# Optimization experiments

Measured on AMD Instinct MI355X. Metric: run time of the kernel, lower is better.

Reference implementation:

```python
import jax, jax.numpy as jnp
import numpy as np

SCALE_CLS = 7.0
EPS = 1e-12

def _l2norm(x):
    # torch F.normalize: x / max(||x||_2, eps) along last dim
    n = jnp.sqrt(jnp.sum(x * x, axis=-1, keepdims=True))
    return x / jnp.maximum(n, EPS)

def setup_inputs() -> dict:
    key = jax.random.key(0)
    k1, k2 = jax.random.split(key)
    B, Q, C, D, H, W = 4, 75, 5, 512, 6, 6
    ftrain = jax.random.normal(k1, (B, Q, C, D, H, W), dtype=jnp.float32)
    ftest = jax.random.normal(k2, (B, Q, C, D, H, W), dtype=jnp.float32)
    return {"ftrain": ftrain, "ftest": ftest, "K": 28}

def reference(ftrain, ftest, K):
    B, Q, C, D, H, W = ftrain.shape
    P = H * W  # 36 spatial positions
    # spatial means -> [B,Q,C,1,D]
    ftest_mean = ftest.mean(axis=(4, 5))[:, :, :, None, :]
    ftrain_mean = ftrain.mean(axis=(4, 5))[:, :, :, None, :]
    # flatten spatial, move channel last -> [B,Q,C,P,D]
    ft = jnp.swapaxes(ftest.reshape(B, Q, C, D, P), 3, 4)
    fr = jnp.swapaxes(ftrain.reshape(B, Q, C, D, P), 3, 4)
    ft = _l2norm(ft)
    fr = _l2norm(fr)
    ftest_mean = _l2norm(ftest_mean)
    ftrain_mean = _l2norm(ftrain_mean)
    # global scores [B,Q,C]
    scores = SCALE_CLS * jnp.sum(jnp.squeeze(ftest_mean * ftrain_mean), axis=-1)
    # per-position scores [B,Q,C,P]
    ftrain_scores = SCALE_CLS * jnp.sum(ftest_mean * fr, axis=-1)
    ftest_scores = SCALE_CLS * jnp.sum(ft * ftrain_mean, axis=-1)
    # top-K positions (indices distinct, so one-hot-sum mask == gather)
    _, train_ind = jax.lax.top_k(ftrain_scores, K)  # [B,Q,C,K]
    _, test_ind = jax.lax.top_k(ftest_scores, K)
    # gather top-K spatial features and average -> [B,Q,C,D]
    ftest_fuse = jnp.take_along_axis(ft, test_ind[..., None], axis=3).sum(axis=3) / K
    ftrain_fuse = jnp.take_along_axis(fr, train_ind[..., None], axis=3).sum(axis=3) / K
    ftest_fuse = _l2norm(ftest_fuse)
    ftrain_fuse = _l2norm(ftrain_fuse)
    scores_final = SCALE_CLS * jnp.sum(ftest_fuse * ftrain_fuse, axis=-1)
    return (scores, scores_final)
```

## Files before the change

### kernel.cpp

```cpp
#include <hip/hip_runtime.h>
#include <stdint.h>

#define NGRP 1500
#define DD   512
#define PP   36
#define DP   (DD*PP)
#define SCALE_CLS 7.0f
#define EPS 1e-12f

__device__ __forceinline__ float waveRed(float x){
  #pragma unroll
  for (int off = 32; off; off >>= 1) x += __shfl_xor(x, off, 64);
  return x;
}

__global__ __launch_bounds__(512)
void topk_fuse(const float* __restrict__ gtrain,
               const float* __restrict__ gtest,
               const int* __restrict__ Kp,
               float* __restrict__ out)
{
  __shared__ float sT[DP];
  __shared__ float sR[DP];
  __shared__ float s_tm[DD], s_rm[DD];
  __shared__ __align__(16) float s_q[PP];
  __shared__ __align__(16) float s_e[PP];
  __shared__ __align__(16) float s_a[PP];
  __shared__ __align__(16) float s_b[PP];
  __shared__ __align__(16) float s_wt[PP];
  __shared__ __align__(16) float s_wr[PP];
  __shared__ float s_nt[PP], s_nr[PP];
  __shared__ float s_st[PP], s_sr[PP];
  __shared__ float s_red[24];

  const int t    = threadIdx.x;
  const int lane = t & 63;
  const int wave = t >> 6;
  const int g    = blockIdx.x;
  const int K    = Kp[0];

  const char* gT = (const char*)(gtest  + (size_t)g * DP);
  const char* gR = (const char*)(gtrain + (size_t)g * DP);
  char* sTc = (char*)sT;
  char* sRc = (char*)sR;

  if (t < PP) { s_q[t] = 0.f; s_e[t] = 0.f; s_a[t] = 0.f; s_b[t] = 0.f; }

  {
    const int base = wave * 9216;
    #pragma unroll
    for (int s = 0; s < 9; ++s) {
      const int off = base + s * 1024;
      __builtin_amdgcn_global_load_lds((const uint32_t*)(gT + off + lane*16),
                                       (uint32_t*)(sTc + off), 16, 0, 0);
    }
    #pragma unroll
    for (int s = 0; s < 9; ++s) {
      const int off = base + s * 1024;
      __builtin_amdgcn_global_load_lds((const uint32_t*)(gR + off + lane*16),
                                       (uint32_t*)(sRc + off), 16, 0, 0);
    }
  }

  asm volatile("s_waitcnt vmcnt(9) lgkmcnt(0)" ::: "memory");
  __builtin_amdgcn_s_barrier();
  __builtin_amdgcn_sched_barrier(0);

  float tm;
  {
    const float4* r4 = (const float4*)(sT + t * PP);
    float s = 0.f;
    #pragma unroll
    for (int j = 0; j < 9; ++j) {
      float4 x = r4[j];
      s += (x.x + x.y) + (x.z + x.w);
    }
    tm = s * (1.0f / 36.0f);
    s_tm[t] = tm;
  }
  {
    float pm2 = waveRed(tm * tm);
    if (lane == 0) s_red[wave] = pm2;
  }

  if (t < 504) {
    const int p = t % 36, c = t / 36;
    float q = 0.f;
    for (int d = c; d < DD; d += 14) { float x = sT[d*PP + p]; q += x * x; }
    atomicAdd(&s_q[p], q);
  }

  asm volatile("s_waitcnt vmcnt(0) lgkmcnt(0)" ::: "memory");
  __builtin_amdgcn_s_barrier();
  __builtin_amdgcn_sched_barrier(0);

  float rm;
  {
    const float4* r4 = (const float4*)(sR + t * PP);
    float s = 0.f;
    #pragma unroll
    for (int j = 0; j < 9; ++j) {
      float4 x = r4[j];
      s += (x.x + x.y) + (x.z + x.w);
    }
    rm = s * (1.0f / 36.0f);
    s_rm[t] = rm;
  }
  {
    float pr2 = waveRed(rm * rm);
    float pmr = waveRed(rm * tm);
    if (lane == 0) { s_red[8 + wave] = pr2; s_red[16 + wave] = pmr; }
  }
  __syncthreads();

  if (t == 0) {
    float m2 = 0.f, r2 = 0.f, mr = 0.f;
    #pragma unroll
    for (int w = 0; w < 8; ++w) {
      m2 += s_red[w]; r2 += s_red[8 + w]; mr += s_red[16 + w];
    }
    out[g] = SCALE_CLS * mr / (fmaxf(sqrtf(m2), EPS) * fmaxf(sqrtf(r2), EPS));
  }

  if (t < 504) {
    const int p = t % 36, c = t / 36;
    float a = 0.f, e = 0.f, b = 0.f;
    for (int d = c; d < DD; d += 14) {
      const int i = d * PP + p;
      float x = sT[i], y = sR[i];
      a += x * s_rm[d];
      e += y * y;
      b += y * s_tm[d];
    }
    atomicAdd(&s_a[p], a); atomicAdd(&s_e[p], e); atomicAdd(&s_b[p], b);
  }
  __syncthreads();

  if (wave < 2 && lane < PP) {
    const float* qq = wave ? s_e : s_q;
    const float* dm = wave ? s_b : s_a;
    float n  = fmaxf(sqrtf(qq[lane]), EPS);
    float sc = dm[lane] / n;
    if (wave) { s_nr[lane] = n; s_sr[lane] = sc; }
    else      { s_nt[lane] = n; s_st[lane] = sc; }
  }
  __syncthreads();

  if (wave < 2 && lane < PP) {
    const float* sc = wave ? s_sr : s_st;
    const float* nn = wave ? s_nr : s_nt;
    float*       w  = wave ? s_wr : s_wt;
    float mine = sc[lane];
    int rank = 0;
    #pragma unroll
    for (int p = 0; p < PP; ++p) {
      float o = sc[p];
      rank += ((o > mine) || (o == mine && p < lane)) ? 1 : 0;
    }
    w[lane] = (rank < K) ? (1.0f / nn[lane]) : 0.f;
  }
  __syncthreads();

  {
    const float4* rt = (const float4*)(sT + t * PP);
    const float4* rr = (const float4*)(sR + t * PP);
    const float4* w4t = (const float4*)s_wt;
    const float4* w4r = (const float4*)s_wr;
    float U = 0.f, V = 0.f;
    #pragma unroll
    for (int j = 0; j < 9; ++j) {
      float4 x = rt[j], y = rr[j], a4 = w4t[j], b4 = w4r[j];
      U += x.x*a4.x + x.y*a4.y + x.z*a4.z + x.w*a4.w;
      V += y.x*b4.x + y.y*b4.y + y.z*b4.z + y.w*b4.w;
    }
    float u2 = waveRed(U * U);
    float v2 = waveRed(V * V);
    float uv = waveRed(U * V);
    if (lane == 0) { s_red[wave] = u2; s_red[8 + wave] = v2; s_red[16 + wave] = uv; }
  }
  __syncthreads();
  if (t == 0) {
    float u2 = 0.f, v2 = 0.f, uv = 0.f;
    #pragma unroll
    for (int w = 0; w < 8; ++w) {
      u2 += s_red[w]; v2 += s_red[8 + w]; uv += s_red[16 + w];
    }
    out[NGRP + g] = SCALE_CLS * uv / (fmaxf(sqrtf(u2), EPS) * fmaxf(sqrtf(v2), EPS));
  }
}

extern "C" void kernel_launch(void* const* d_in, const int* in_sizes, int n_in,
                              void* d_out, int out_size, void* d_ws, size_t ws_size,
                              hipStream_t stream)
{
  const float* ftrain = (const float*)d_in[0];
  const float* ftest  = (const float*)d_in[1];
  const int*   Kp     = (const int*)d_in[2];
  float*       out    = (float*)d_out;
  topk_fuse<<<NGRP, 512, 0, stream>>>(ftrain, ftest, Kp, out);
}
```

Measured before the change: 271.3 us.

## Use persistent blocks with register prefetch of next group's features

Replaces one-block-per-group launch with 256 persistent blocks that loop over groups, prefetching the next group's test and train tiles into registers while computing the current one from LDS. It also merges the per-position norm and dot reductions into one pass and computes both means together. The aim is to hide global-memory latency behind compute, since LDS usage allows only one block per CU. In exchange it uses many registers per thread and adds an explicit register-to-LDS copy each iteration.

```diff
diff --git a/kernel.cpp b/kernel.cpp
--- a/kernel.cpp
+++ b/kernel.cpp
@@ -5,6 +5,9 @@
 #define DD   512
 #define PP   36
 #define DP   (DD*PP)
+#define NB   256
+#define NT   512
+#define QPT  9
 #define SCALE_CLS 7.0f
 #define EPS 1e-12f
 
@@ -14,178 +17,149 @@
   return x;
 }
 
-__global__ __launch_bounds__(512)
-void topk_fuse(const float* __restrict__ gtrain,
-               const float* __restrict__ gtest,
-               const int* __restrict__ Kp,
-               float* __restrict__ out)
+__global__ __launch_bounds__(NT, 2)
+void topk_fuse(const float* gtrain, const float* gtest,
+               const int* Kp, float* out)
 {
   __shared__ float sT[DP];
   __shared__ float sR[DP];
   __shared__ float s_tm[DD], s_rm[DD];
-  __shared__ __align__(16) float s_q[PP];
-  __shared__ __align__(16) float s_e[PP];
-  __shared__ __align__(16) float s_a[PP];
-  __shared__ __align__(16) float s_b[PP];
+  __shared__ float s_q[PP], s_e[PP];
+  __shared__ float s_a[PP], s_b[PP];
+  __shared__ float s_nt[PP], s_nr[PP];
+  __shared__ float s_st[PP], s_sr[PP];
   __shared__ __align__(16) float s_wt[PP];
   __shared__ __align__(16) float s_wr[PP];
-  __shared__ float s_nt[PP], s_nr[PP];
-  __shared__ float s_st[PP], s_sr[PP];
   __shared__ float s_red[24];
 
   const int t    = threadIdx.x;
   const int lane = t & 63;
   const int wave = t >> 6;
-  const int g    = blockIdx.x;
+  const int b    = blockIdx.x;
   const int K    = Kp[0];
+  const int nj   = (NGRP - b + NB - 1) / NB;
 
-  const char* gT = (const char*)(gtest  + (size_t)g * DP);
-  const char* gR = (const char*)(gtrain + (size_t)g * DP);
-  char* sTc = (char*)sT;
-  char* sRc = (char*)sR;
-
+  float4 pT[QPT], pR[QPT];
+  {
+    const float4* gT4 = (const float4*)(gtest  + (size_t)b * DP);
+    const float4* gR4 = (const float4*)(gtrain + (size_t)b * DP);
+    #pragma unroll
+    for (int s = 0; s < QPT; ++s) pT[s] = gT4[t + NT*s];
+    #pragma unroll
+    for (int s = 0; s < QPT; ++s) pR[s] = gR4[t + NT*s];
+  }
   if (t < PP) { s_q[t] = 0.f; s_e[t] = 0.f; s_a[t] = 0.f; s_b[t] = 0.f; }
 
-  {
-    const int base = wave * 9216;
+  for (int j = 0; j < nj; ++j) {
+    const int g = b + NB * j;
+
+    float4* sT4 = (float4*)sT;
+    float4* sR4 = (float4*)sR;
     #pragma unroll
-    for (int s = 0; s < 9; ++s) {
-      const int off = base + s * 1024;
-      __builtin_amdgcn_global_load_lds((const uint32_t*)(gT + off + lane*16),
-                                       (uint32_t*)(sTc + off), 16, 0, 0);
+    for (int s = 0; s < QPT; ++s) sT4[t + NT*s] = pT[s];
+    #pragma unroll
+    for (int s = 0; s < QPT; ++s) sR4[t + NT*s] = pR[s];
+
+    if (j + 1 < nj) {
+      const int g2 = g + NB;
+      const float4* gT4 = (const float4*)(gtest  + (size_t)g2 * DP);
+      const float4* gR4 = (const float4*)(gtrain + (size_t)g2 * DP);
+      #pragma unroll
+      for (int s = 0; s < QPT; ++s) pT[s] = gT4[t + NT*s];
+      #pragma unroll
+      for (int s = 0; s < QPT; ++s) pR[s] = gR4[t + NT*s];
     }
+    __builtin_amdgcn_sched_barrier(0);
+    __syncthreads();
+
+    const float4* rt4 = (const float4*)(sT + t * PP);
+    const float4* rr4 = (const float4*)(sR + t * PP);
+    float st = 0.f, sr = 0.f;
     #pragma unroll
-    for (int s = 0; s < 9; ++s) {
-      const int off = base + s * 1024;
-      __builtin_amdgcn_global_load_lds((const uint32_t*)(gR + off + lane*16),
-                                       (uint32_t*)(sRc + off), 16, 0, 0);
+    for (int i = 0; i < 9; ++i) {
+      float4 x = rt4[i], y = rr4[i];
+      st += (x.x + x.y) + (x.z + x.w);
+      sr += (y.x + y.y) + (y.z + y.w);
     }
-  }
+    const float tm = st * (1.0f/36.0f), rm = sr * (1.0f/36.0f);
+    s_tm[t] = tm; s_rm[t] = rm;
+    {
+      float pm2 = waveRed(tm * tm);
+      float pr2 = waveRed(rm * rm);
+      float pmr = waveRed(tm * rm);
+      if (lane == 0) { s_red[wave] = pm2; s_red[8+wave] = pr2; s_red[16+wave] = pmr; }
+    }
+    __syncthreads();
 
-  asm volatile("s_waitcnt vmcnt(9) lgkmcnt(0)" ::: "memory");
-  __builtin_amdgcn_s_barrier();
-  __builtin_amdgcn_sched_barrier(0);
+    if (t == 0) {
+      float m2 = 0.f, r2 = 0.f, mr = 0.f;
+      #pragma unroll
+      for (int w = 0; w < 8; ++w) { m2 += s_red[w]; r2 += s_red[8+w]; mr += s_red[16+w]; }
+      out[g] = SCALE_CLS * mr / (fmaxf(sqrtf(m2), EPS) * fmaxf(sqrtf(r2), EPS));
+    }
 
-  float tm;
-  {
-    const float4* r4 = (const float4*)(sT + t * PP);
-    float s = 0.f;
-    #pragma unroll
-    for (int j = 0; j < 9; ++j) {
-      float4 x = r4[j];
-      s += (x.x + x.y) + (x.z + x.w);
+    if (t < 504) {
+      const int p = t % 36, c = t / 36;
+      float q = 0.f, e = 0.f, a = 0.f, bb = 0.f;
+      for (int d = c; d < DD; d += 14) {
+        const int i = d * PP + p;
+        float x = sT[i], y = sR[i];
+        q += x * x;        e += y * y;
+        a += x * s_rm[d];  bb += y * s_tm[d];
+      }
+      atomicAdd(&s_q[p], q);  atomicAdd(&s_e[p], e);
+      atomicAdd(&s_a[p], a);  atomicAdd(&s_b[p], bb);
     }
-    tm = s * (1.0f / 36.0f);
-    s_tm[t] = tm;
-  }
-  {
-    float pm2 = waveRed(tm * tm);
-    if (lane == 0) s_red[wave] = pm2;
-  }
+    __syncthreads();
 
-  if (t < 504) {
-    const int p = t % 36, c = t / 36;
-    float q = 0.f;
-    for (int d = c; d < DD; d += 14) { float x = sT[d*PP + p]; q += x * x; }
-    atomicAdd(&s_q[p], q);
-  }
+    if (wave < 2 && lane < PP) {
+      const float* qq = wave ? s_e : s_q;
+      const float* dm = wave ? s_b : s_a;
+      float n  = fmaxf(sqrtf(qq[lane]), EPS);
+      float sc = dm[lane] / n;
+      if (wave) { s_nr[lane] = n; s_sr[lane] = sc; }
+      else      { s_nt[lane] = n; s_st[lane] = sc; }
+    }
+    __syncthreads();
 
-  asm volatile("s_waitcnt vmcnt(0) lgkmcnt(0)" ::: "memory");
-  __builtin_amdgcn_s_barrier();
-  __builtin_amdgcn_sched_barrier(0);
+    if (wave < 2 && lane < PP) {
+      const float* sc = wave ? s_sr : s_st;
+      const float* nn = wave ? s_nr : s_nt;
+      float*       w  = wave ? s_wr : s_wt;
+      float mine = sc[lane];
+      int rank = 0;
+      #pragma unroll
+      for (int p = 0; p < PP; ++p) {
+        float o = sc[p];
+        rank += ((o > mine) || (o == mine && p < lane)) ? 1 : 0;
+      }
+      w[lane] = (rank < K) ? (1.0f / nn[lane]) : 0.f;
+    }
+    if (wave == 2 && lane < PP) { s_q[lane]=0.f; s_e[lane]=0.f; s_a[lane]=0.f; s_b[lane]=0.f; }
+    __syncthreads();
 
-  float rm;
-  {
-    const float4* r4 = (const float4*)(sR + t * PP);
-    float s = 0.f;
-    #pragma unroll
-    for (int j = 0; j < 9; ++j) {
-      float4 x = r4[j];
-      s += (x.x + x.y) + (x.z + x.w);
+    {
+      const float4* w4t = (const float4*)s_wt;
+      const float4* w4r = (const float4*)s_wr;
+      float U = 0.f, V = 0.f;
+      #pragma unroll
+      for (int i = 0; i < 9; ++i) {
+        float4 x = rt4[i], y = rr4[i], wa = w4t[i], wb = w4r[i];
+        U += x.x*wa.x + x.y*wa.y + x.z*wa.z + x.w*wa.w;
+        V += y.x*wb.x + y.y*wb.y + y.z*wb.z + y.w*wb.w;
+      }
+      float u2 = waveRed(U * U);
+      float v2 = waveRed(V * V);
+      float uv = waveRed(U * V);
+      if (lane == 0) { s_red[wave] = u2; s_red[8+wave] = v2; s_red[16+wave] = uv; }
     }
-    rm = s * (1.0f / 36.0f);
-    s_rm[t] = rm;
-  }
-  {
-    float pr2 = waveRed(rm * rm);
-    float pmr = waveRed(rm * tm);
-    if (lane == 0) { s_red[8 + wave] = pr2; s_red[16 + wave] = pmr; }
-  }
-  __syncthreads();
-
-  if (t == 0) {
-    float m2 = 0.f, r2 = 0.f, mr = 0.f;
-    #pragma unroll
-    for (int w = 0; w < 8; ++w) {
-      m2 += s_red[w]; r2 += s_red[8 + w]; mr += s_red[16 + w];
+    __syncthreads();
+    if (t == 0) {
+      float u2 = 0.f, v2 = 0.f, uv = 0.f;
+      #pragma unroll
+      for (int w = 0; w < 8; ++w) { u2 += s_red[w]; v2 += s_red[8+w]; uv += s_red[16+w]; }
+      out[NGRP + g] = SCALE_CLS * uv / (fmaxf(sqrtf(u2), EPS) * fmaxf(sqrtf(v2), EPS));
     }
-    out[g] = SCALE_CLS * mr / (fmaxf(sqrtf(m2), EPS) * fmaxf(sqrtf(r2), EPS));
-  }
-
-  if (t < 504) {
-    const int p = t % 36, c = t / 36;
-    float a = 0.f, e = 0.f, b = 0.f;
-    for (int d = c; d < DD; d += 14) {
-      const int i = d * PP + p;
-      float x = sT[i], y = sR[i];
-      a += x * s_rm[d];
-      e += y * y;
-      b += y * s_tm[d];
-    }
-    atomicAdd(&s_a[p], a); atomicAdd(&s_e[p], e); atomicAdd(&s_b[p], b);
-  }
-  __syncthreads();
-
-  if (wave < 2 && lane < PP) {
-    const float* qq = wave ? s_e : s_q;
-    const float* dm = wave ? s_b : s_a;
-    float n  = fmaxf(sqrtf(qq[lane]), EPS);
-    float sc = dm[lane] / n;
-    if (wave) { s_nr[lane] = n; s_sr[lane] = sc; }
-    else      { s_nt[lane] = n; s_st[lane] = sc; }
-  }
-  __syncthreads();
-
-  if (wave < 2 && lane < PP) {
-    const float* sc = wave ? s_sr : s_st;
-    const float* nn = wave ? s_nr : s_nt;
-    float*       w  = wave ? s_wr : s_wt;
-    float mine = sc[lane];
-    int rank = 0;
-    #pragma unroll
-    for (int p = 0; p < PP; ++p) {
-      float o = sc[p];
-      rank += ((o > mine) || (o == mine && p < lane)) ? 1 : 0;
-    }
-    w[lane] = (rank < K) ? (1.0f / nn[lane]) : 0.f;
-  }
-  __syncthreads();
-
-  {
-    const float4* rt = (const float4*)(sT + t * PP);
-    const float4* rr = (const float4*)(sR + t * PP);
-    const float4* w4t = (const float4*)s_wt;
-    const float4* w4r = (const float4*)s_wr;
-    float U = 0.f, V = 0.f;
-    #pragma unroll
-    for (int j = 0; j < 9; ++j) {
-      float4 x = rt[j], y = rr[j], a4 = w4t[j], b4 = w4r[j];
-      U += x.x*a4.x + x.y*a4.y + x.z*a4.z + x.w*a4.w;
-      V += y.x*b4.x + y.y*b4.y + y.z*b4.z + y.w*b4.w;
-    }
-    float u2 = waveRed(U * U);
-    float v2 = waveRed(V * V);
-    float uv = waveRed(U * V);
-    if (lane == 0) { s_red[wave] = u2; s_red[8 + wave] = v2; s_red[16 + wave] = uv; }
-  }
-  __syncthreads();
-  if (t == 0) {
-    float u2 = 0.f, v2 = 0.f, uv = 0.f;
-    #pragma unroll
-    for (int w = 0; w < 8; ++w) {
-      u2 += s_red[w]; v2 += s_red[8 + w]; uv += s_red[16 + w];
-    }
-    out[NGRP + g] = SCALE_CLS * uv / (fmaxf(sqrtf(u2), EPS) * fmaxf(sqrtf(v2), EPS));
   }
 }
 
@@ -197,5 +171,5 @@
   const float* ftest  = (const float*)d_in[1];
   const int*   Kp     = (const int*)d_in[2];
   float*       out    = (float*)d_out;
-  topk_fuse<<<NGRP, 512, 0, stream>>>(ftrain, ftest, Kp, out);
+  topk_fuse<<<NB, NT, 0, stream>>>(ftrain, ftest, Kp, out);
 }
```

New measurement: 342.3 us. +26.2%, slower.
